# Optimization experiments

Hardware: AMD Instinct MI355X
Metric: run time of the kernel (lower is better)

The kernel has to match this reference:

```python
import jax, jax.numpy as jnp
import numpy as np

D = 512      # d_model
NH = 8       # n_heads
P = 7        # n_points
B = 1        # forced by the module's broadcast/view (only valid for B==1)
H0 = 128
W0 = 128
N = H0 * W0


def setup_inputs() -> dict:
    key = jax.random.key(0)
    ks = jax.random.split(key, 12)
    s = 0.02
    f32 = jnp.float32
    return {
        "x": jax.random.normal(ks[0], (B, N, D), f32),
        "H": H0,
        "W": W0,
        "Wq": jax.random.normal(ks[1], (D, D), f32) * s,
        "bq": jnp.zeros((D,), f32),
        "Wk": jax.random.normal(ks[2], (D, D), f32) * s,
        "bk": jnp.zeros((D,), f32),
        "Wv": jax.random.normal(ks[3], (D, D), f32) * s,
        "bv": jnp.zeros((D,), f32),
        "Wo": jax.random.normal(ks[4], (D, D), f32) * s,
        "bo": jnp.zeros((D,), f32),
        "Woff1": jax.random.normal(ks[5], (D, D), f32) * s,
        "boff1": jnp.zeros((D,), f32),
        "Woff2": jax.random.normal(ks[6], (D, 2 * P), f32) * s,
        "boff2": jnp.zeros((2 * P,), f32),
    }


def reference(x, H, W, Wq, bq, Wk, bk, Wv, bv, Wo, bo, Woff1, boff1, Woff2, boff2):
    Bx, Nx, Dm = x.shape
    nH = NH
    hd = Dm // nH
    p = Woff2.shape[1] // 2

    # projections -> (B, nH, N, hd)
    q = (x @ Wq + bq).reshape(Bx, Nx, nH, hd).transpose(0, 2, 1, 3)
    k = (x @ Wk + bk).reshape(Bx, Nx, nH, hd).transpose(0, 2, 1, 3)
    v = (x @ Wv + bv).reshape(Bx, Nx, nH, hd).transpose(0, 2, 1, 3)

    # per-token offsets (B, N, p, 2), shared across heads (as in the torch module)
    off = jnp.tanh(jax.nn.relu(x @ Woff1 + boff1) @ Woff2 + boff2)
    off = off.reshape(Bx, Nx, p, 2)

    # base integer grid coords, stacked as (x, y) to match torch
    cy = jnp.repeat(jnp.arange(H), W)            # (N,)
    cx = jnp.tile(jnp.arange(W), H)              # (N,)
    coords = jnp.stack([cx, cy], axis=-1).astype(x.dtype)  # (N, 2)

    samp = coords[None, :, None, :] + off * (2.0 / max(H, W))  # (B, N, p, 2)
    ix = jnp.clip(jnp.round(samp[..., 0]), 0, W - 1).astype(jnp.int32)
    iy = jnp.clip(jnp.round(samp[..., 1]), 0, H - 1).astype(jnp.int32)
    idx = (iy * W + ix).reshape(Bx, 1, Nx * p, 1)  # broadcast over heads & hd

    # irregular gather of K/V at sampled locations -> (B, nH, N, p, hd)
    k_s = jnp.take_along_axis(k, idx, axis=2).reshape(Bx, nH, Nx, p, hd)
    v_s = jnp.take_along_axis(v, idx, axis=2).reshape(Bx, nH, Nx, p, hd)

    inv_sqrt = (1.0 / np.sqrt(hd)).astype(np.float32)
    scores = jnp.einsum('bhnd,bhnpd->bhnp', q, k_s) * inv_sqrt
    attn = jax.nn.softmax(scores, axis=-1)  # dropout is identity in eval
    out_h = jnp.einsum('bhnp,bhnpd->bhnd', attn, v_s)
    out = out_h.transpose(0, 2, 1, 3).reshape(Bx, Nx, Dm) @ Wo + bo
    return out
```

## Files before the change

kernel.cpp:

```cpp
#include <hip/hip_runtime.h>
#include <hip/hip_bf16.h>
#include <stdint.h>


typedef unsigned short u16;
typedef short bf16x8 __attribute__((ext_vector_type(8)));
typedef u16 ushort8 __attribute__((ext_vector_type(8)));
typedef float f32x4 __attribute__((ext_vector_type(4)));

__device__ __forceinline__ u16 f2bf(float f) {
  __hip_bfloat16 h = __float2bfloat16(f);
  union { __hip_bfloat16 h; u16 u; } v; v.h = h; return v.u;
}

#define WS_WPT 0
#define WS_P   524288

__global__ void ws_probe(int* p) {
  if (blockIdx.x == 7 && threadIdx.x == 0) p[0] = 0;
}

__global__ __launch_bounds__(256)
void precompose_fused(const float* __restrict__ Wv, const float* __restrict__ bv,
                      const float* __restrict__ Wo, u16* __restrict__ WpT,
                      float* __restrict__ P) {
  const int b = blockIdx.x;
  const int tid = threadIdx.x;

  if (b >= 64) {
    const int j = b - 64;
    const int n = tid;
    float s0 = 0.f, s1 = 0.f;
#pragma unroll
    for (int mm = 0; mm < 8; ++mm) {
      const float bvm = bv[8 * j + mm];
      const float* w = Wo + (size_t)(8 * j + mm) * 512;
      s0 += bvm * w[n];
      s1 += bvm * w[n + 256];
    }
    P[(size_t)j * 512 + n] = s0;
    P[(size_t)j * 512 + n + 256] = s1;
    return;
  }

  __shared__ u16 As[64 * 72];
  __shared__ u16 Bs[64 * 72];
  const int lane = tid & 63, wave = tid >> 6;
  const int wm = wave & 1, wn = wave >> 1;
  const int q = lane >> 4, lr = lane & 15;
  const int i0 = (b >> 3) * 64;
  const int j0 = (b & 7) * 64;

  f32x4 acc[2][2];
#pragma unroll
  for (int i = 0; i < 2; ++i)
#pragma unroll
    for (int j = 0; j < 2; ++j) { f32x4 z = {0.f,0.f,0.f,0.f}; acc[i][j] = z; }

  for (int m0 = 0; m0 < 512; m0 += 64) {
#pragma unroll
    for (int su = 0; su < 16; ++su) {
      const int s = su * 256 + tid;
      const int mloc = s >> 6, nloc = s & 63;
      As[nloc * 72 + mloc] = f2bf(Wo[(size_t)(m0 + mloc) * 512 + i0 + nloc]);
    }
#pragma unroll
    for (int su = 0; su < 2; ++su) {
      const int s = su * 256 + tid;
      const int row = s >> 3, p = s & 7;
      const float* sv = Wv + (size_t)(j0 + row) * 512 + m0 + p * 8;
      f32x4 a = *(const f32x4*)sv, c4 = *(const f32x4*)(sv + 4);
      ushort8 o;
      o[0]=f2bf(a[0]); o[1]=f2bf(a[1]); o[2]=f2bf(a[2]); o[3]=f2bf(a[3]);
      o[4]=f2bf(c4[0]); o[5]=f2bf(c4[1]); o[6]=f2bf(c4[2]); o[7]=f2bf(c4[3]);
      *(ushort8*)(Bs + row * 72 + p * 8) = o;
    }
    __syncthreads();

#pragma unroll
    for (int kk = 0; kk < 2; ++kk) {
      const int c = kk * 4 + q;
      bf16x8 af[2], bfr[2];
#pragma unroll
      for (int t = 0; t < 2; ++t) {
        af[t]  = *(const bf16x8*)(As + (wm * 32 + t * 16 + lr) * 72 + c * 8);
        bfr[t] = *(const bf16x8*)(Bs + (wn * 32 + t * 16 + lr) * 72 + c * 8);
      }
#pragma unroll
      for (int mt = 0; mt < 2; ++mt)
#pragma unroll
        for (int nt = 0; nt < 2; ++nt)
          acc[mt][nt] = __builtin_amdgcn_mfma_f32_16x16x32_bf16(
              af[mt], bfr[nt], acc[mt][nt], 0, 0, 0);
    }
    __syncthreads();
  }

#pragma unroll
  for (int nt = 0; nt < 2; ++nt) {
    const int col = j0 + wn * 32 + nt * 16 + lr;
#pragma unroll
    for (int mt = 0; mt < 2; ++mt) {
      const int row0 = i0 + wm * 32 + mt * 16 + q * 4;
#pragma unroll
      for (int r = 0; r < 4; ++r)
        WpT[(size_t)(row0 + r) * 512 + col] = f2bf(acc[mt][nt][r]);
    }
  }
}

__global__ __launch_bounds__(256, 2)
void gemm_x_bt(const float* __restrict__ x, const u16* __restrict__ BT,
               const float* __restrict__ P, const float* __restrict__ bo,
               float* __restrict__ C) {
  constexpr int BM = 128, BK = 64;
  __shared__ u16 As[BM * BK];
  __shared__ u16 Bs[BM * BK];
  __shared__ float bias_s[BM];

  const int tid = threadIdx.x;
  const int lane = tid & 63, wave = tid >> 6;
  const int wm = wave & 1, wn = wave >> 1;
  const int q = lane >> 4, lr = lane & 15;
  const int m0 = blockIdx.x * BM;
  const int n0 = blockIdx.y * BM;

  if (tid < 128) {
    float s = bo[n0 + tid];
#pragma unroll 8
    for (int j = 0; j < 64; ++j) s += P[(size_t)j * 512 + n0 + tid];
    bias_s[tid] = s;
  }

  f32x4 acc[4][4];
#pragma unroll
  for (int i = 0; i < 4; ++i)
#pragma unroll
    for (int j = 0; j < 4; ++j) { f32x4 z = {0.f,0.f,0.f,0.f}; acc[i][j] = z; }

  f32x4 pa0[4], pa1[4];
  ushort8 pb[4];

  auto load_tile = [&](int k0) {
#pragma unroll
    for (int it = 0; it < 4; ++it) {
      const int s = it * 256 + tid;
      const int row = s >> 3, p = s & 7;
      const int c = p ^ (row & 7);
      const float* sx = x + (size_t)(m0 + row) * 512 + k0 + c * 8;
      pa0[it] = *(const f32x4*)sx;
      pa1[it] = *(const f32x4*)(sx + 4);
      pb[it] = *(const ushort8*)(BT + (size_t)(n0 + row) * 512 + k0 + c * 8);
    }
  };
  auto store_tile = [&]() {
#pragma unroll
    for (int it = 0; it < 4; ++it) {
      const int s = it * 256 + tid;
      ushort8 o;
      o[0]=f2bf(pa0[it][0]); o[1]=f2bf(pa0[it][1]);
      o[2]=f2bf(pa0[it][2]); o[3]=f2bf(pa0[it][3]);
      o[4]=f2bf(pa1[it][0]); o[5]=f2bf(pa1[it][1]);
      o[6]=f2bf(pa1[it][2]); o[7]=f2bf(pa1[it][3]);
      *(ushort8*)(As + s * 8) = o;
      *(ushort8*)(Bs + s * 8) = pb[it];
    }
  };
  auto compute = [&]() {
#pragma unroll
    for (int kk = 0; kk < 2; ++kk) {
      const int c = kk * 4 + q;
      bf16x8 af[4], bfr[4];
#pragma unroll
      for (int t = 0; t < 4; ++t) {
        const int rowA = wm * 64 + t * 16 + lr;
        af[t] = *(const bf16x8*)(As + rowA * BK + (c ^ (rowA & 7)) * 8);
        const int rowB = wn * 64 + t * 16 + lr;
        bfr[t] = *(const bf16x8*)(Bs + rowB * BK + (c ^ (rowB & 7)) * 8);
      }
#pragma unroll
      for (int mt = 0; mt < 4; ++mt)
#pragma unroll
        for (int nt = 0; nt < 4; ++nt)
          acc[mt][nt] = __builtin_amdgcn_mfma_f32_16x16x32_bf16(
              af[mt], bfr[nt], acc[mt][nt], 0, 0, 0);
    }
  };

  load_tile(0);
  store_tile();
  __syncthreads();
  for (int k0 = 64; k0 < 512; k0 += 64) {
    load_tile(k0);
    compute();
    __syncthreads();
    store_tile();
    __syncthreads();
  }
  compute();

#pragma unroll
  for (int nt = 0; nt < 4; ++nt) {
    const int lcol = wn * 64 + nt * 16 + lr;
    const float bsv = bias_s[lcol];
#pragma unroll
    for (int mt = 0; mt < 4; ++mt) {
      const int grow0 = m0 + wm * 64 + mt * 16 + q * 4;
#pragma unroll
      for (int r = 0; r < 4; ++r)
        C[(size_t)(grow0 + r) * 512 + n0 + lcol] = acc[mt][nt][r] + bsv;
    }
  }
}

extern "C" void kernel_launch(void* const* d_in, const int* in_sizes, int n_in,
                              void* d_out, int out_size, void* d_ws, size_t ws_size,
                              hipStream_t stream) {
  const float* x  = (const float*)d_in[0];
  const float* Wv = (const float*)d_in[7];
  const float* bv = (const float*)d_in[8];
  const float* Wo = (const float*)d_in[9];
  const float* bo = (const float*)d_in[10];
  float* outp = (float*)d_out;

  u16*   WpT = (u16*)((uint8_t*)d_ws + WS_WPT);
  float* P   = (float*)((uint8_t*)d_ws + WS_P);

  int wsmb = (int)(ws_size >> 20); if (wsmb > 896) wsmb = 896;
  ws_probe<<<1, 64 + wsmb, 0, stream>>>((int*)d_ws);

  precompose_fused<<<128, 256, 0, stream>>>(Wv, bv, Wo, WpT, P);
  gemm_x_bt<<<dim3(128, 4), 256, 0, stream>>>(x, WpT, P, bo, outp);
}
```

Before: 134.0 us.

## Double-buffer GEMM LDS tiles with async B loads and drop probe launch

The GEMM main loop now uses two LDS buffers. The B tile (bf16 WpT) is copied straight from global memory to LDS with global_load_lds, and the next A tile is loaded and stored into the alternate buffer while the current one is being computed. This removes one barrier per k-step and the register staging for B. The bias reduction is moved after the first tile loads are issued so it overlaps them. The extra ws_probe kernel launch is removed. LDS use doubles to 64KB per block, which may limit occupancy, and correctness depends on the async LDS writes being complete before the barrier.

Measured after the change: 135.2 us. No clear change (+0.9%).

```diff
diff --git a/kernel.cpp b/kernel.cpp
--- a/kernel.cpp
+++ b/kernel.cpp
@@ -13,12 +13,14 @@
   union { __hip_bfloat16 h; u16 u; } v; v.h = h; return v.u;
 }
 
+__device__ __forceinline__ void async_copy16(const void* g, void* lds) {
+  __builtin_amdgcn_global_load_lds(
+      (const __attribute__((address_space(1))) uint32_t*)g,
+      (__attribute__((address_space(3))) uint32_t*)lds, 16, 0, 0);
+}
+
 #define WS_WPT 0
 #define WS_P   524288
-
-__global__ void ws_probe(int* p) {
-  if (blockIdx.x == 7 && threadIdx.x == 0) p[0] = 0;
-}
 
 __global__ __launch_bounds__(256)
 void precompose_fused(const float* __restrict__ Wv, const float* __restrict__ bv,
@@ -114,8 +116,8 @@
                const float* __restrict__ P, const float* __restrict__ bo,
                float* __restrict__ C) {
   constexpr int BM = 128, BK = 64;
-  __shared__ u16 As[BM * BK];
-  __shared__ u16 Bs[BM * BK];
+  __shared__ u16 As[2][BM * BK];
+  __shared__ u16 Bs[2][BM * BK];
   __shared__ float bias_s[BM];
 
   const int tid = threadIdx.x;
@@ -125,13 +127,6 @@
   const int m0 = blockIdx.x * BM;
   const int n0 = blockIdx.y * BM;
 
-  if (tid < 128) {
-    float s = bo[n0 + tid];
-#pragma unroll 8
-    for (int j = 0; j < 64; ++j) s += P[(size_t)j * 512 + n0 + tid];
-    bias_s[tid] = s;
-  }
-
   f32x4 acc[4][4];
 #pragma unroll
   for (int i = 0; i < 4; ++i)
@@ -139,9 +134,19 @@
     for (int j = 0; j < 4; ++j) { f32x4 z = {0.f,0.f,0.f,0.f}; acc[i][j] = z; }
 
   f32x4 pa0[4], pa1[4];
-  ushort8 pb[4];
-
-  auto load_tile = [&](int k0) {
+
+  auto asyncB = [&](int k0, int buf) {
+#pragma unroll
+    for (int it = 0; it < 4; ++it) {
+      const int sbase = it * 256 + wave * 64;
+      const int s = sbase + lane;
+      const int row = s >> 3, p = s & 7;
+      const int c = p ^ (row & 7);
+      async_copy16(BT + (size_t)(n0 + row) * 512 + k0 + c * 8,
+                   &Bs[buf][sbase * 8]);
+    }
+  };
+  auto loadA = [&](int k0) {
 #pragma unroll
     for (int it = 0; it < 4; ++it) {
       const int s = it * 256 + tid;
@@ -150,10 +155,9 @@
       const float* sx = x + (size_t)(m0 + row) * 512 + k0 + c * 8;
       pa0[it] = *(const f32x4*)sx;
       pa1[it] = *(const f32x4*)(sx + 4);
-      pb[it] = *(const ushort8*)(BT + (size_t)(n0 + row) * 512 + k0 + c * 8);
-    }
-  };
-  auto store_tile = [&]() {
+    }
+  };
+  auto storeA = [&](int buf) {
 #pragma unroll
     for (int it = 0; it < 4; ++it) {
       const int s = it * 256 + tid;
@@ -162,11 +166,10 @@
       o[2]=f2bf(pa0[it][2]); o[3]=f2bf(pa0[it][3]);
       o[4]=f2bf(pa1[it][0]); o[5]=f2bf(pa1[it][1]);
       o[6]=f2bf(pa1[it][2]); o[7]=f2bf(pa1[it][3]);
-      *(ushort8*)(As + s * 8) = o;
-      *(ushort8*)(Bs + s * 8) = pb[it];
-    }
-  };
-  auto compute = [&]() {
+      *(ushort8*)(&As[buf][s * 8]) = o;
+    }
+  };
+  auto compute = [&](int buf) {
 #pragma unroll
     for (int kk = 0; kk < 2; ++kk) {
       const int c = kk * 4 + q;
@@ -174,9 +177,9 @@
 #pragma unroll
       for (int t = 0; t < 4; ++t) {
         const int rowA = wm * 64 + t * 16 + lr;
-        af[t] = *(const bf16x8*)(As + rowA * BK + (c ^ (rowA & 7)) * 8);
+        af[t] = *(const bf16x8*)(&As[buf][rowA * BK + ((c ^ (rowA & 7)) * 8)]);
         const int rowB = wn * 64 + t * 16 + lr;
-        bfr[t] = *(const bf16x8*)(Bs + rowB * BK + (c ^ (rowB & 7)) * 8);
+        bfr[t] = *(const bf16x8*)(&Bs[buf][rowB * BK + ((c ^ (rowB & 7)) * 8)]);
       }
 #pragma unroll
       for (int mt = 0; mt < 4; ++mt)
@@ -187,17 +190,27 @@
     }
   };
 
-  load_tile(0);
-  store_tile();
+  asyncB(0, 0);
+  loadA(0);
+  if (tid < 128) {
+    float s = bo[n0 + tid];
+#pragma unroll 8
+    for (int j = 0; j < 64; ++j) s += P[(size_t)j * 512 + n0 + tid];
+    bias_s[tid] = s;
+  }
+  storeA(0);
   __syncthreads();
-  for (int k0 = 64; k0 < 512; k0 += 64) {
-    load_tile(k0);
-    compute();
+
+  int cur = 0;
+  for (int k = 1; k < 8; ++k) {
+    asyncB(k * 64, cur ^ 1);
+    loadA(k * 64);
+    compute(cur);
+    storeA(cur ^ 1);
     __syncthreads();
-    store_tile();
-    __syncthreads();
-  }
-  compute();
+    cur ^= 1;
+  }
+  compute(cur);
 
 #pragma unroll
   for (int nt = 0; nt < 4; ++nt) {
@@ -226,9 +239,6 @@
   u16*   WpT = (u16*)((uint8_t*)d_ws + WS_WPT);
   float* P   = (float*)((uint8_t*)d_ws + WS_P);
 
-  int wsmb = (int)(ws_size >> 20); if (wsmb > 896) wsmb = 896;
-  ws_probe<<<1, 64 + wsmb, 0, stream>>>((int*)d_ws);
-
   precompose_fused<<<128, 256, 0, stream>>>(Wv, bv, Wo, WpT, P);
   gemm_x_bt<<<dim3(128, 4), 256, 0, stream>>>(x, WpT, P, bo, outp);
 }
```
